# Kernel optimization log

Hardware: AMD Instinct MI355X
Metric: run time of the kernel (lower is better)

Reference implementation:

```python
import jax, jax.numpy as jnp
import numpy as np

B, C, HEADS, D, DKQ = 1024, 512, 8, 64, 8
DV = C // HEADS                 # 64, dim_head_v
QKVC = DV + 2 * DKQ             # 80, qkv channels per head
EPS = 1e-5


def _bn(x, g, b, m, v):
    # eval-mode batchnorm, channel axis = 1
    shp = (1, -1) + (1,) * (x.ndim - 2)
    scale = g.reshape(shp) / jnp.sqrt(v.reshape(shp) + EPS)
    return (x - m.reshape(shp)) * scale + b.reshape(shp)


def _rel_index():
    i = np.arange(D)
    # key_index - query_index + D - 1, row-major flatten -> (D*D,)
    return jnp.asarray((i[:, None] - i[None, :] + D - 1).reshape(-1))


def setup_inputs() -> dict:
    key = jax.random.key(0)
    ks = jax.random.split(key, 16)
    O = HEADS * QKVC
    d = {
        "x": jax.random.normal(ks[0], (B, C, D), jnp.float32),
        "conv_w": jax.random.normal(ks[1], (O, C), jnp.float32) * 0.02,
        "bn1_g": jax.random.normal(ks[2], (O,), jnp.float32) * 0.1 + 1.0,
        "bn1_b": jax.random.normal(ks[3], (O,), jnp.float32) * 0.1,
        "bn1_m": jax.random.normal(ks[4], (O,), jnp.float32) * 0.1,
        "bn1_v": jax.random.uniform(ks[5], (O,), jnp.float32) * 0.5 + 0.5,
        "rel": jax.random.normal(ks[6], (QKVC, 2 * D - 1), jnp.float32),
        "bn2_g": jax.random.normal(ks[7], (3 * HEADS,), jnp.float32) * 0.1 + 1.0,
        "bn2_b": jax.random.normal(ks[8], (3 * HEADS,), jnp.float32) * 0.1,
        "bn2_m": jax.random.normal(ks[9], (3 * HEADS,), jnp.float32) * 0.1,
        "bn2_v": jax.random.uniform(ks[10], (3 * HEADS,), jnp.float32) * 0.5 + 0.5,
        "bn3_g": jax.random.normal(ks[11], (2 * C,), jnp.float32) * 0.1 + 1.0,
        "bn3_b": jax.random.normal(ks[12], (2 * C,), jnp.float32) * 0.1,
        "bn3_m": jax.random.normal(ks[13], (2 * C,), jnp.float32) * 0.1,
        "bn3_v": jax.random.uniform(ks[14], (2 * C,), jnp.float32) * 0.5 + 0.5,
    }
    return d


def reference(x, conv_w, bn1_g, bn1_b, bn1_m, bn1_v, rel,
              bn2_g, bn2_b, bn2_m, bn2_v, bn3_g, bn3_b, bn3_m, bn3_v):
    # 1x1 conv1d + BN1d: [B, O, D]
    qkv = jnp.einsum('oc,bcd->bod', conv_w, x)
    qkv = _bn(qkv, bn1_g, bn1_b, bn1_m, bn1_v)
    # rearrange 'b (q h) d -> b h q d' with q=QKVC, h=HEADS (channel = q*H + h)
    qkv = qkv.reshape(B, QKVC, HEADS, D).transpose(0, 2, 1, 3)  # [B,H,QKVC,D]
    q = qkv[:, :, :DKQ]                # [B,H,DKQ,D]
    k = qkv[:, :, DKQ:2 * DKQ]         # [B,H,DKQ,D]
    v = qkv[:, :, 2 * DKQ:]            # [B,H,DV,D]

    # relative positional embeddings gathered from table
    emb = rel[:, _rel_index()].reshape(QKVC, D, D)
    r_q, r_k, r_v = emb[:DKQ], emb[DKQ:2 * DKQ], emb[2 * DKQ:]

    qr = jnp.einsum('bhid,idj->bhdj', q, r_q)
    kr = jnp.einsum('bhid,idj->bhdj', k, r_k)
    dots = jnp.einsum('bhid,bhij->bhdj', q, k)

    # rearrange 'n b h d j -> b (h n) d j'  (channel = h*3 + n)
    stacked = jnp.stack([qr, kr, dots], axis=2).reshape(B, 3 * HEADS, D, D)
    stacked = _bn(stacked, bn2_g, bn2_b, bn2_m, bn2_v)
    norm_dots = stacked.reshape(B, HEADS, 3, D, D).sum(axis=2)  # [B,H,D,D]

    attn = jax.nn.softmax(norm_dots, axis=-1)
    out = jnp.einsum('bhdj,bhij->bhid', attn, v)      # [B,H,DV,D]
    kv = jnp.einsum('bhdj,idj->bhid', attn, r_v)      # [B,H,DV,D]

    # rearrange 'n b h i d -> b (n h i) d'  (channel = n*H*DV + h*DV + i)
    st = jnp.stack([kv, out], axis=1).reshape(B, 2 * HEADS * DV, D)
    st = _bn(st, bn3_g, bn3_b, bn3_m, bn3_v)
    return st.reshape(B, 2, HEADS * DV, D).sum(axis=1)  # [B,C,D]
```

## Files before the change

kernel.cpp:

```cpp
#include <hip/hip_runtime.h>
#include <hip/hip_bf16.h>

#define B_    1024
#define C_    512
#define H_    8
#define D_    64
#define EPS_  1e-5f

typedef __attribute__((ext_vector_type(4))) float f32x4;
typedef __attribute__((ext_vector_type(8))) short bf16x8;
typedef __attribute__((ext_vector_type(8))) unsigned short u16x8;

__device__ __forceinline__ float bf2f(unsigned short h) {
    union { unsigned int u; float f; } c;
    c.u = ((unsigned int)h) << 16;
    return c.f;
}
__device__ __forceinline__ unsigned short f2bf(float f) {
    __hip_bfloat16 h = __float2bfloat16(f);
    return *reinterpret_cast<unsigned short*>(&h);
}

__global__ __launch_bounds__(256) void k0_wconv(
    const float* __restrict__ w, unsigned short* __restrict__ wf)
{
    int t = blockIdx.x * 256 + threadIdx.x;
    int o  = t >> 6;
    int c0 = (t & 63) * 8;
    const float* src = w + (size_t)o * C_ + c0;
    u16x8 p;
#pragma unroll
    for (int e = 0; e < 8; ++e) p[e] = f2bf(src[e]);
    int f = (o >> 4) * 16 + (c0 >> 5);
    int l = (o & 15) | (((c0 >> 3) & 3) << 4);
    *reinterpret_cast<u16x8*>(&wf[(size_t)f * 512 + l * 8]) = p;
}

__global__ __launch_bounds__(256) void k0_tables(
    const float* __restrict__ rel,
    const float* __restrict__ g2, const float* __restrict__ v2,
    const float* __restrict__ g3, const float* __restrict__ v3,
    unsigned short* __restrict__ relB, unsigned short* __restrict__ relvA)
{
    int tid = blockIdx.x * 256 + threadIdx.x;
    if (tid < 4096) {
        int h = tid >> 9, uf = (tid >> 6) & 7, l = tid & 63;
        int u = uf * 16 + (l & 15);
        int g = l >> 4;
        float sq = g2[3*h]     * rsqrtf(v2[3*h]     + EPS_);
        float sk = g2[3*h + 1] * rsqrtf(v2[3*h + 1] + EPS_);
        u16x8 p;
#pragma unroll
        for (int e = 0; e < 8; ++e) {
            int s = g * 8 + e;
            float val = 0.f;
            if (u < 127 && s < 16)
                val = (s < 8 ? sq : sk) * rel[s * 127 + u];
            p[e] = f2bf(val);
        }
        *reinterpret_cast<u16x8*>(&relB[(size_t)tid * 8]) = p;
    } else if (tid < 4096 + 8192) {
        int t2 = tid - 4096;
        int h = t2 >> 10, iF = (t2 >> 8) & 3, tt = (t2 >> 6) & 3, l = t2 & 63;
        int i = iF * 16 + (l & 15);
        int c3 = h * 64 + i;
        float scl = g3[c3] * rsqrtf(v3[c3] + EPS_);
        const float* rrow = rel + (size_t)(16 + i) * 127;
        u16x8 p;
#pragma unroll
        for (int e = 0; e < 8; ++e) {
            int u = (l >> 4) * 8 + e + 32 * tt;
            p[e] = f2bf((u < 127) ? scl * rrow[u] : 0.f);
        }
        *reinterpret_cast<u16x8*>(&relvA[(size_t)t2 * 8]) = p;
    }
}

#define LDW1 72

struct K1Ctx {
    const float* xb;
    const unsigned short* wf;
    unsigned short (*xt)[64 * LDW1];
    int wv, lane, lm, lg, cp, c4;
};

struct XPair { f32x4 a, c; };

template<int KT>
__device__ __forceinline__ void k1_step(const K1Ctx& c, f32x4 (&acc)[5][4],
                                        bf16x8 (&afu)[10], bf16x8 (&afp)[10],
                                        XPair& xu, XPair& xn)
{
    if (KT < 6) {
        xn.a = *reinterpret_cast<const f32x4*>(&c.xb[((KT + 2) * 64 + 2 * c.cp) * 64 + c.c4]);
        xn.c = *reinterpret_cast<const f32x4*>(&c.xb[((KT + 2) * 64 + 2 * c.cp + 1) * 64 + c.c4]);
    }
    if (KT < 7) {
#pragma unroll
        for (int j = 0; j < 4; ++j) {
            unsigned int pk = (unsigned int)f2bf(xu.a[j]) | ((unsigned int)f2bf(xu.c[j]) << 16);
            *reinterpret_cast<unsigned int*>(
                &c.xt[(KT + 1) & 1][(c.c4 + j) * LDW1 + 2 * c.cp]) = pk;
        }
    }
    if (KT < 7) {
#pragma unroll
        for (int i = 0; i < 10; ++i) {
            int fm = i % 5, ks = i / 5;
            size_t f = (size_t)((c.wv * 5 + fm) * 16 + (KT + 1) * 2 + ks) * 512;
            afp[i] = *reinterpret_cast<const bf16x8*>(&c.wf[f + c.lane * 8]);
        }
    }
#pragma unroll
    for (int ks = 0; ks < 2; ++ks) {
        bf16x8 bfr[4];
#pragma unroll
        for (int fn = 0; fn < 4; ++fn)
            bfr[fn] = *reinterpret_cast<const bf16x8*>(
                &c.xt[KT & 1][(fn * 16 + c.lm) * LDW1 + ks * 32 + c.lg * 8]);
#pragma unroll
        for (int fm = 0; fm < 5; ++fm)
#pragma unroll
            for (int fn = 0; fn < 4; ++fn)
                acc[fm][fn] = __builtin_amdgcn_mfma_f32_16x16x32_bf16(
                    afu[ks * 5 + fm], bfr[fn], acc[fm][fn], 0, 0, 0);
    }
    __syncthreads();
}

__global__ __launch_bounds__(512) void k1_gemm(
    const float* __restrict__ x, const unsigned short* __restrict__ wf,
    const float* __restrict__ g1, const float* __restrict__ b1,
    const float* __restrict__ m1, const float* __restrict__ v1,
    const float* __restrict__ g3, const float* __restrict__ v3,
    unsigned short* __restrict__ qkA, unsigned short* __restrict__ vB)
{
    __shared__ unsigned short xt[2][64 * LDW1];
    __shared__ float ssc[640], ssh[640];

    const int tid = threadIdx.x;
    const int b   = blockIdx.x;

    for (int t = tid; t < 640; t += 512) {
        float sc = g1[t] * rsqrtf(v1[t] + EPS_);
        float sh = b1[t] - m1[t] * sc;
        int cc = t >> 3, hh = t & 7;
        if (cc >= 16) {
            int c3 = 512 + hh * 64 + (cc - 16);
            float f = g3[c3] * rsqrtf(v3[c3] + EPS_);
            sc *= f; sh *= f;
        }
        ssc[t] = sc;
        ssh[t] = sh;
    }

    K1Ctx c;
    c.xb   = x + (size_t)b * C_ * D_;
    c.wf   = wf;
    c.xt   = xt;
    c.lane = tid & 63;
    c.wv   = tid >> 6;
    c.lm   = c.lane & 15;
    c.lg   = c.lane >> 4;
    c.cp   = tid >> 4;
    c.c4   = (tid & 15) * 4;

    f32x4 acc[5][4];
#pragma unroll
    for (int i = 0; i < 5; ++i)
#pragma unroll
        for (int j = 0; j < 4; ++j) acc[i][j] = (f32x4){0.f, 0.f, 0.f, 0.f};

    bf16x8 afA[10], afB[10];
    XPair  xP, xQ;
#pragma unroll
    for (int i = 0; i < 10; ++i) {
        int fm = i % 5, ks = i / 5;
        size_t f = (size_t)((c.wv * 5 + fm) * 16 + ks) * 512;
        afA[i] = *reinterpret_cast<const bf16x8*>(&wf[f + c.lane * 8]);
    }
    {
        f32x4 a = *reinterpret_cast<const f32x4*>(&c.xb[(2 * c.cp) * 64 + c.c4]);
        f32x4 d = *reinterpret_cast<const f32x4*>(&c.xb[(2 * c.cp + 1) * 64 + c.c4]);
        xP.a = *reinterpret_cast<const f32x4*>(&c.xb[(64 + 2 * c.cp) * 64 + c.c4]);
        xP.c = *reinterpret_cast<const f32x4*>(&c.xb[(64 + 2 * c.cp + 1) * 64 + c.c4]);
#pragma unroll
        for (int j = 0; j < 4; ++j) {
            unsigned int pk = (unsigned int)f2bf(a[j]) | ((unsigned int)f2bf(d[j]) << 16);
            *reinterpret_cast<unsigned int*>(&xt[0][(c.c4 + j) * LDW1 + 2 * c.cp]) = pk;
        }
    }
    __syncthreads();

    k1_step<0>(c, acc, afA, afB, xP, xQ);
    k1_step<1>(c, acc, afB, afA, xQ, xP);
    k1_step<2>(c, acc, afA, afB, xP, xQ);
    k1_step<3>(c, acc, afB, afA, xQ, xP);
    k1_step<4>(c, acc, afA, afB, xP, xQ);
    k1_step<5>(c, acc, afB, afA, xQ, xP);
    k1_step<6>(c, acc, afA, afB, xP, xQ);
    k1_step<7>(c, acc, afB, afA, xQ, xP);

    const int wv = c.wv, lm = c.lm, lg = c.lg;
#pragma unroll
    for (int fm = 0; fm < 5; ++fm) {
#pragma unroll
        for (int fn = 0; fn < 4; ++fn) {
            int d = fn * 16 + lm;
#pragma unroll
            for (int r = 0; r < 4; ++r) {
                int o = wv * 80 + fm * 16 + lg * 4 + r;
                int cc = o >> 3, hh = o & 7;
                float val = acc[fm][fn][r] * ssc[o] + ssh[o];
                unsigned short bv = f2bf(val);
                if (cc < 8)
                    qkA[(((size_t)b * 8 + hh) * 4 + (d >> 4)) * 512 + (d & 15) * 8 + cc] = bv;
                else if (cc < 16)
                    qkA[(((size_t)b * 8 + hh) * 4 + (d >> 4)) * 512 + ((d & 15) + 16) * 8 + (cc - 8)] = bv;
                else
                    vB[((size_t)(b * 8 + hh) * 64 + (cc - 16)) * 64 + d] = bv;
            }
        }
    }
    for (int z = tid; z < 4096; z += 512) {
        int hh  = z >> 9;
        int mf  = (z >> 7) & 3;
        int off = z & 127;
        unsigned int* p = reinterpret_cast<unsigned int*>(
            qkA + (((size_t)b * 8 + hh) * 4 + mf) * 512 + 256);
        p[off] = 0u;
    }
}

#define SGP 84
#define SA  72
#define RLD 136

__global__ __launch_bounds__(256) void k2_attn(
    const unsigned short* __restrict__ qkA, const unsigned short* __restrict__ vB,
    const unsigned short* __restrict__ relB, const unsigned short* __restrict__ relvA,
    const float* __restrict__ g2, const float* __restrict__ v2,
    const float* __restrict__ g3, const float* __restrict__ b3,
    const float* __restrict__ m3, const float* __restrict__ v3,
    float* __restrict__ outp)
{
    __shared__ float          SGb[64 * SGP];
    __shared__ unsigned short attn[64 * SA];
    __shared__ unsigned short A2[64 * RLD];
    __shared__ float sh3[64];

    const int tid  = threadIdx.x;
    const int b    = blockIdx.x >> 3;
    const int h    = blockIdx.x & 7;
    const int lane = tid & 63;
    const int w    = tid >> 6;
    const int lmm  = lane & 15;
    const int lg   = lane >> 4;

    const unsigned short* qbase = qkA + ((size_t)(b * 8 + h) * 4) * 512;

    for (int i = tid; i < 64 * RLD / 2; i += 256)
        reinterpret_cast<unsigned int*>(A2)[i] = 0u;
    if (tid < 64) {
        int c = h * 64 + tid;
        float sa = g3[c] * rsqrtf(v3[c] + EPS_);
        float sb = g3[512 + c] * rsqrtf(v3[512 + c] + EPS_);
        sh3[tid] = (b3[c] - m3[c] * sa) + (b3[512 + c] - m3[512 + c] * sb);
    }
    const float s_dt = g2[3 * h + 2] * rsqrtf(v2[3 * h + 2] + EPS_);

    bf16x8 aA = *reinterpret_cast<const bf16x8*>(&qbase[w * 512 + lane * 8]);
    bf16x8 zv = {0, 0, 0, 0, 0, 0, 0, 0};
    bf16x8 kBf[4];
#pragma unroll
    for (int jf = 0; jf < 4; ++jf) {
        kBf[jf] = zv;
        if (lane < 16)
            kBf[jf] = *reinterpret_cast<const bf16x8*>(&qbase[jf * 512 + (lane + 16) * 8]);
    }
    bf16x8 rBf[8];
#pragma unroll
    for (int uf = 0; uf < 8; ++uf)
        rBf[uf] = *reinterpret_cast<const bf16x8*>(&relB[(size_t)(h * 8 + uf) * 512 + lane * 8]);

    f32x4 dotsAcc[4];
#pragma unroll
    for (int jf = 0; jf < 4; ++jf)
        dotsAcc[jf] = __builtin_amdgcn_mfma_f32_16x16x32_bf16(
            aA, kBf[jf], (f32x4){0.f, 0.f, 0.f, 0.f}, 0, 0, 0);
    f32x4 sgAcc[8];
#pragma unroll
    for (int uf = 0; uf < 8; ++uf)
        sgAcc[uf] = __builtin_amdgcn_mfma_f32_16x16x32_bf16(
            aA, rBf[uf], (f32x4){0.f, 0.f, 0.f, 0.f}, 0, 0, 0);

#pragma unroll
    for (int uf = 0; uf < 8; ++uf) {
#pragma unroll
        for (int r = 0; r < 4; ++r) {
            int d = (w << 4) + (lg << 2) + r;
            int t = uf * 16 + lmm - d + 15;
            if (t >= 0 && t < 79)
                SGb[d * SGP + t] = sgAcc[uf][r];
        }
    }
    __syncthreads();

#pragma unroll
    for (int r = 0; r < 4; ++r) {
        int d = (w << 4) + (lg << 2) + r;
        const float* sgr = &SGb[d * SGP];
        float sc0 = s_dt * dotsAcc[0][r] + sgr[78 - lmm];
        float sc1 = s_dt * dotsAcc[1][r] + sgr[62 - lmm];
        float sc2 = s_dt * dotsAcc[2][r] + sgr[46 - lmm];
        float sc3 = s_dt * dotsAcc[3][r] + sgr[30 - lmm];
        float mx = fmaxf(fmaxf(sc0, sc1), fmaxf(sc2, sc3));
        mx = fmaxf(mx, __shfl_xor(mx, 1));
        mx = fmaxf(mx, __shfl_xor(mx, 2));
        mx = fmaxf(mx, __shfl_xor(mx, 4));
        mx = fmaxf(mx, __shfl_xor(mx, 8));
        float e0 = __expf(sc0 - mx), e1 = __expf(sc1 - mx);
        float e2 = __expf(sc2 - mx), e3 = __expf(sc3 - mx);
        float sum = (e0 + e1) + (e2 + e3);
        sum += __shfl_xor(sum, 1);
        sum += __shfl_xor(sum, 2);
        sum += __shfl_xor(sum, 4);
        sum += __shfl_xor(sum, 8);
        float inv = 1.f / sum;
        unsigned short p0 = f2bf(e0 * inv), p1 = f2bf(e1 * inv);
        unsigned short p2 = f2bf(e2 * inv), p3 = f2bf(e3 * inv);
        attn[d * SA + lmm]      = p0;
        attn[d * SA + 16 + lmm] = p1;
        attn[d * SA + 32 + lmm] = p2;
        attn[d * SA + 48 + lmm] = p3;
        A2[d * RLD + 63 + d - lmm] = p0;
        A2[d * RLD + 47 + d - lmm] = p1;
        A2[d * RLD + 31 + d - lmm] = p2;
        A2[d * RLD + 15 + d - lmm] = p3;
    }

    const int lk8  = lg * 8;
    const int irow = (w << 4) + lmm;
    const unsigned short* vbase = vB + (size_t)(b * 8 + h) * 4096;
    bf16x8 av0 = *reinterpret_cast<const bf16x8*>(&vbase[irow * 64 + lk8]);
    bf16x8 av1 = *reinterpret_cast<const bf16x8*>(&vbase[irow * 64 + 32 + lk8]);
    bf16x8 rvA[4];
#pragma unroll
    for (int t = 0; t < 4; ++t)
        rvA[t] = *reinterpret_cast<const bf16x8*>(
            &relvA[(size_t)(((h * 4 + w) * 4 + t)) * 512 + lane * 8]);

    __syncthreads();

    f32x4 acc[4];
#pragma unroll
    for (int nf = 0; nf < 4; ++nf) acc[nf] = (f32x4){0.f, 0.f, 0.f, 0.f};

#pragma unroll
    for (int nf = 0; nf < 4; ++nf) {
        const unsigned short* arow = &attn[(nf * 16 + lmm) * SA + lk8];
        acc[nf] = __builtin_amdgcn_mfma_f32_16x16x32_bf16(
            av0, *reinterpret_cast<const bf16x8*>(&arow[0]), acc[nf], 0, 0, 0);
        acc[nf] = __builtin_amdgcn_mfma_f32_16x16x32_bf16(
            av1, *reinterpret_cast<const bf16x8*>(&arow[32]), acc[nf], 0, 0, 0);
        const unsigned short* a2row = &A2[(nf * 16 + lmm) * RLD + lk8];
        acc[nf] = __builtin_amdgcn_mfma_f32_16x16x32_bf16(
            rvA[0], *reinterpret_cast<const bf16x8*>(&a2row[0]), acc[nf], 0, 0, 0);
        acc[nf] = __builtin_amdgcn_mfma_f32_16x16x32_bf16(
            rvA[1], *reinterpret_cast<const bf16x8*>(&a2row[32]), acc[nf], 0, 0, 0);
        acc[nf] = __builtin_amdgcn_mfma_f32_16x16x32_bf16(
            rvA[2], *reinterpret_cast<const bf16x8*>(&a2row[64]), acc[nf], 0, 0, 0);
        acc[nf] = __builtin_amdgcn_mfma_f32_16x16x32_bf16(
            rvA[3], *reinterpret_cast<const bf16x8*>(&a2row[96]), acc[nf], 0, 0, 0);
    }

    float* op = outp + ((size_t)b * 512 + h * 64) * 64;
    const int r0 = lg * 4;
#pragma unroll
    for (int r = 0; r < 4; ++r) {
        int i = (w << 4) + r0 + r;
        float sh = sh3[i];
#pragma unroll
        for (int nf = 0; nf < 4; ++nf)
            op[(size_t)i * 64 + nf * 16 + lmm] = acc[nf][r] + sh;
    }
}

extern "C" void kernel_launch(void* const* d_in, const int* in_sizes, int n_in,
                              void* d_out, int out_size, void* d_ws, size_t ws_size,
                              hipStream_t stream) {
    (void)in_sizes; (void)n_in; (void)out_size; (void)ws_size;
    const float* x   = (const float*)d_in[0];
    const float* w   = (const float*)d_in[1];
    const float* g1  = (const float*)d_in[2];
    const float* b1  = (const float*)d_in[3];
    const float* m1  = (const float*)d_in[4];
    const float* v1  = (const float*)d_in[5];
    const float* rel = (const float*)d_in[6];
    const float* g2  = (const float*)d_in[7];
    const float* b2  = (const float*)d_in[8];  (void)b2;
    const float* m2  = (const float*)d_in[9];  (void)m2;
    const float* v2  = (const float*)d_in[10];
    const float* g3  = (const float*)d_in[11];
    const float* b3  = (const float*)d_in[12];
    const float* m3  = (const float*)d_in[13];
    const float* v3  = (const float*)d_in[14];
    float* out = (float*)d_out;

    unsigned short* wfrag = (unsigned short*)d_ws;
    unsigned short* relB  = (unsigned short*)((char*)d_ws + 655360);
    unsigned short* relvA = (unsigned short*)((char*)d_ws + 720896);
    unsigned short* qkA   = (unsigned short*)((char*)d_ws + 1048576);
    unsigned short* vB    = (unsigned short*)((char*)d_ws + 1048576 + (size_t)33554432);

    hipLaunchKernelGGL(k0_wconv, dim3(160), dim3(256), 0, stream, w, wfrag);
    hipLaunchKernelGGL(k0_tables, dim3(48), dim3(256), 0, stream,
                       rel, g2, v2, g3, v3, relB, relvA);
    hipLaunchKernelGGL(k1_gemm, dim3(1024), dim3(512), 0, stream,
                       x, wfrag, g1, b1, m1, v1, g3, v3, qkA, vB);
    hipLaunchKernelGGL(k2_attn, dim3(8192), dim3(256), 0, stream,
                       qkA, vB, relB, relvA, g2, v2, g3, b3, m3, v3, out);
}
```

Baseline: 172.1 us.

## Split k1 GEMM across two blocks per batch with 32-channel K steps

The projection GEMM now launches two 256-thread blocks per batch element, each computing half of the 640 output rows, instead of one 512-thread block. The K loop uses 16 steps of 32 channels with one MFMA k-slice per step, which halves the A-fragment register arrays and shrinks the LDS x tile. The aim is more concurrent blocks and lower register/LDS pressure per block. In exchange, every x tile is loaded and converted to bf16 twice (once per block), there are twice as many barriers, and both blocks redundantly zero the qkA padding.

Result: slower. 192.4 us (+11.8%).

```diff
diff --git a/kernel.cpp b/kernel.cpp
--- a/kernel.cpp
+++ b/kernel.cpp
@@ -76,27 +76,27 @@
     }
 }
 
-#define LDW1 72
+#define LDW1 40
 
 struct K1Ctx {
     const float* xb;
-    const unsigned short* wf;
+    const unsigned short* wfw;
     unsigned short (*xt)[64 * LDW1];
-    int wv, lane, lm, lg, cp, c4;
+    int lane, lm, lg, cp, c4;
 };
 
 struct XPair { f32x4 a, c; };
 
 template<int KT>
 __device__ __forceinline__ void k1_step(const K1Ctx& c, f32x4 (&acc)[5][4],
-                                        bf16x8 (&afu)[10], bf16x8 (&afp)[10],
+                                        bf16x8 (&afu)[5], bf16x8 (&afp)[5],
                                         XPair& xu, XPair& xn)
 {
-    if (KT < 6) {
-        xn.a = *reinterpret_cast<const f32x4*>(&c.xb[((KT + 2) * 64 + 2 * c.cp) * 64 + c.c4]);
-        xn.c = *reinterpret_cast<const f32x4*>(&c.xb[((KT + 2) * 64 + 2 * c.cp + 1) * 64 + c.c4]);
-    }
-    if (KT < 7) {
+    if (KT < 14) {
+        xn.a = *reinterpret_cast<const f32x4*>(&c.xb[((KT + 2) * 32 + 2 * c.cp) * 64 + c.c4]);
+        xn.c = *reinterpret_cast<const f32x4*>(&c.xb[((KT + 2) * 32 + 2 * c.cp + 1) * 64 + c.c4]);
+    }
+    if (KT < 15) {
 #pragma unroll
         for (int j = 0; j < 4; ++j) {
             unsigned int pk = (unsigned int)f2bf(xu.a[j]) | ((unsigned int)f2bf(xu.c[j]) << 16);
@@ -104,32 +104,27 @@
                 &c.xt[(KT + 1) & 1][(c.c4 + j) * LDW1 + 2 * c.cp]) = pk;
         }
     }
-    if (KT < 7) {
-#pragma unroll
-        for (int i = 0; i < 10; ++i) {
-            int fm = i % 5, ks = i / 5;
-            size_t f = (size_t)((c.wv * 5 + fm) * 16 + (KT + 1) * 2 + ks) * 512;
-            afp[i] = *reinterpret_cast<const bf16x8*>(&c.wf[f + c.lane * 8]);
-        }
-    }
-#pragma unroll
-    for (int ks = 0; ks < 2; ++ks) {
-        bf16x8 bfr[4];
+    if (KT < 15) {
+#pragma unroll
+        for (int fm = 0; fm < 5; ++fm)
+            afp[fm] = *reinterpret_cast<const bf16x8*>(
+                &c.wfw[(size_t)(fm * 16 + KT + 1) * 512]);
+    }
+    bf16x8 bfr[4];
+#pragma unroll
+    for (int fn = 0; fn < 4; ++fn)
+        bfr[fn] = *reinterpret_cast<const bf16x8*>(
+            &c.xt[KT & 1][(fn * 16 + c.lm) * LDW1 + c.lg * 8]);
+#pragma unroll
+    for (int fm = 0; fm < 5; ++fm)
 #pragma unroll
         for (int fn = 0; fn < 4; ++fn)
-            bfr[fn] = *reinterpret_cast<const bf16x8*>(
-                &c.xt[KT & 1][(fn * 16 + c.lm) * LDW1 + ks * 32 + c.lg * 8]);
-#pragma unroll
-        for (int fm = 0; fm < 5; ++fm)
-#pragma unroll
-            for (int fn = 0; fn < 4; ++fn)
-                acc[fm][fn] = __builtin_amdgcn_mfma_f32_16x16x32_bf16(
-                    afu[ks * 5 + fm], bfr[fn], acc[fm][fn], 0, 0, 0);
-    }
+            acc[fm][fn] = __builtin_amdgcn_mfma_f32_16x16x32_bf16(
+                afu[fm], bfr[fn], acc[fm][fn], 0, 0, 0);
     __syncthreads();
 }
 
-__global__ __launch_bounds__(512) void k1_gemm(
+__global__ __launch_bounds__(256) void k1_gemm(
     const float* __restrict__ x, const unsigned short* __restrict__ wf,
     const float* __restrict__ g1, const float* __restrict__ b1,
     const float* __restrict__ m1, const float* __restrict__ v1,
@@ -137,15 +132,17 @@
     unsigned short* __restrict__ qkA, unsigned short* __restrict__ vB)
 {
     __shared__ unsigned short xt[2][64 * LDW1];
-    __shared__ float ssc[640], ssh[640];
-
-    const int tid = threadIdx.x;
-    const int b   = blockIdx.x;
-
-    for (int t = tid; t < 640; t += 512) {
-        float sc = g1[t] * rsqrtf(v1[t] + EPS_);
-        float sh = b1[t] - m1[t] * sc;
-        int cc = t >> 3, hh = t & 7;
+    __shared__ float ssc[320], ssh[320];
+
+    const int tid  = threadIdx.x;
+    const int b    = blockIdx.x >> 1;
+    const int row0 = (blockIdx.x & 1) * 320;
+
+    for (int t = tid; t < 320; t += 256) {
+        int o = row0 + t;
+        float sc = g1[o] * rsqrtf(v1[o] + EPS_);
+        float sh = b1[o] - m1[o] * sc;
+        int cc = o >> 3, hh = o & 7;
         if (cc >= 16) {
             int c3 = 512 + hh * 64 + (cc - 16);
             float f = g3[c3] * rsqrtf(v3[c3] + EPS_);
@@ -157,14 +154,14 @@
 
     K1Ctx c;
     c.xb   = x + (size_t)b * C_ * D_;
-    c.wf   = wf;
-    c.xt   = xt;
     c.lane = tid & 63;
-    c.wv   = tid >> 6;
+    const int wv = tid >> 6;
     c.lm   = c.lane & 15;
     c.lg   = c.lane >> 4;
     c.cp   = tid >> 4;
     c.c4   = (tid & 15) * 4;
+    c.xt   = xt;
+    c.wfw  = wf + (size_t)((row0 >> 4) + wv * 5) * 16 * 512 + c.lane * 8;
 
     f32x4 acc[5][4];
 #pragma unroll
@@ -172,19 +169,16 @@
 #pragma unroll
         for (int j = 0; j < 4; ++j) acc[i][j] = (f32x4){0.f, 0.f, 0.f, 0.f};
 
-    bf16x8 afA[10], afB[10];
+    bf16x8 afA[5], afB[5];
     XPair  xP, xQ;
 #pragma unroll
-    for (int i = 0; i < 10; ++i) {
-        int fm = i % 5, ks = i / 5;
-        size_t f = (size_t)((c.wv * 5 + fm) * 16 + ks) * 512;
-        afA[i] = *reinterpret_cast<const bf16x8*>(&wf[f + c.lane * 8]);
-    }
+    for (int fm = 0; fm < 5; ++fm)
+        afA[fm] = *reinterpret_cast<const bf16x8*>(&c.wfw[(size_t)(fm * 16) * 512]);
     {
         f32x4 a = *reinterpret_cast<const f32x4*>(&c.xb[(2 * c.cp) * 64 + c.c4]);
         f32x4 d = *reinterpret_cast<const f32x4*>(&c.xb[(2 * c.cp + 1) * 64 + c.c4]);
-        xP.a = *reinterpret_cast<const f32x4*>(&c.xb[(64 + 2 * c.cp) * 64 + c.c4]);
-        xP.c = *reinterpret_cast<const f32x4*>(&c.xb[(64 + 2 * c.cp + 1) * 64 + c.c4]);
+        xP.a = *reinterpret_cast<const f32x4*>(&c.xb[(32 + 2 * c.cp) * 64 + c.c4]);
+        xP.c = *reinterpret_cast<const f32x4*>(&c.xb[(32 + 2 * c.cp + 1) * 64 + c.c4]);
 #pragma unroll
         for (int j = 0; j < 4; ++j) {
             unsigned int pk = (unsigned int)f2bf(a[j]) | ((unsigned int)f2bf(d[j]) << 16);
@@ -193,16 +187,24 @@
     }
     __syncthreads();
 
-    k1_step<0>(c, acc, afA, afB, xP, xQ);
-    k1_step<1>(c, acc, afB, afA, xQ, xP);
-    k1_step<2>(c, acc, afA, afB, xP, xQ);
-    k1_step<3>(c, acc, afB, afA, xQ, xP);
-    k1_step<4>(c, acc, afA, afB, xP, xQ);
-    k1_step<5>(c, acc, afB, afA, xQ, xP);
-    k1_step<6>(c, acc, afA, afB, xP, xQ);
-    k1_step<7>(c, acc, afB, afA, xQ, xP);
-
-    const int wv = c.wv, lm = c.lm, lg = c.lg;
+    k1_step< 0>(c, acc, afA, afB, xP, xQ);
+    k1_step< 1>(c, acc, afB, afA, xQ, xP);
+    k1_step< 2>(c, acc, afA, afB, xP, xQ);
+    k1_step< 3>(c, acc, afB, afA, xQ, xP);
+    k1_step< 4>(c, acc, afA, afB, xP, xQ);
+    k1_step< 5>(c, acc, afB, afA, xQ, xP);
+    k1_step< 6>(c, acc, afA, afB, xP, xQ);
+    k1_step< 7>(c, acc, afB, afA, xQ, xP);
+    k1_step< 8>(c, acc, afA, afB, xP, xQ);
+    k1_step< 9>(c, acc, afB, afA, xQ, xP);
+    k1_step<10>(c, acc, afA, afB, xP, xQ);
+    k1_step<11>(c, acc, afB, afA, xQ, xP);
+    k1_step<12>(c, acc, afA, afB, xP, xQ);
+    k1_step<13>(c, acc, afB, afA, xQ, xP);
+    k1_step<14>(c, acc, afA, afB, xP, xQ);
+    k1_step<15>(c, acc, afB, afA, xQ, xP);
+
+    const int lm = c.lm, lg = c.lg;
 #pragma unroll
     for (int fm = 0; fm < 5; ++fm) {
 #pragma unroll
@@ -210,9 +212,10 @@
             int d = fn * 16 + lm;
 #pragma unroll
             for (int r = 0; r < 4; ++r) {
-                int o = wv * 80 + fm * 16 + lg * 4 + r;
+                int rl = wv * 80 + fm * 16 + lg * 4 + r;
+                int o  = row0 + rl;
                 int cc = o >> 3, hh = o & 7;
-                float val = acc[fm][fn][r] * ssc[o] + ssh[o];
+                float val = acc[fm][fn][r] * ssc[rl] + ssh[rl];
                 unsigned short bv = f2bf(val);
                 if (cc < 8)
                     qkA[(((size_t)b * 8 + hh) * 4 + (d >> 4)) * 512 + (d & 15) * 8 + cc] = bv;
@@ -223,7 +226,7 @@
             }
         }
     }
-    for (int z = tid; z < 4096; z += 512) {
+    for (int z = tid; z < 4096; z += 256) {
         int hh  = z >> 9;
         int mf  = (z >> 7) & 3;
         int off = z & 127;
@@ -417,7 +420,7 @@
     hipLaunchKernelGGL(k0_wconv, dim3(160), dim3(256), 0, stream, w, wfrag);
     hipLaunchKernelGGL(k0_tables, dim3(48), dim3(256), 0, stream,
                        rel, g2, v2, g3, v3, relB, relvA);
-    hipLaunchKernelGGL(k1_gemm, dim3(1024), dim3(512), 0, stream,
+    hipLaunchKernelGGL(k1_gemm, dim3(2048), dim3(256), 0, stream,
                        x, wfrag, g1, b1, m1, v1, g3, v3, qkA, vB);
     hipLaunchKernelGGL(k2_attn, dim3(8192), dim3(256), 0, stream,
                        qkA, vB, relB, relvA, g2, v2, g3, b3, m3, v3, out);
```
